# Optimization experiments

Hardware: AMD Instinct MI355X
Metric: run time of the kernel (lower is better)

## Reference

```python
import jax, jax.numpy as jnp
import numpy as np

B, T = 64, 32
F_DIM, V = 1024, 4000
H = V  # hidden_size == vocab_size in the module


def setup_inputs() -> dict:
    key = jax.random.key(0)
    ks = jax.random.split(key, 10)
    s = 1.0 / np.sqrt(H)  # torch LSTM init: U(-1/sqrt(H), 1/sqrt(H))
    u = lambda k, shp: jax.random.uniform(k, shp, jnp.float32, -s, s)
    return {
        "features": jax.random.normal(ks[0], (B, F_DIM), jnp.float32),
        "captions": jax.random.randint(ks[1], (B, T), 0, V, jnp.int32),
        "W_ih0": u(ks[2], (4 * H, F_DIM + V)),
        "W_hh0": u(ks[3], (4 * H, H)),
        "b_ih0": u(ks[4], (4 * H,)),
        "b_hh0": u(ks[5], (4 * H,)),
        "W_ih1": u(ks[6], (4 * H, H)),
        "W_hh1": u(ks[7], (4 * H, H)),
        "b_ih1": u(ks[8], (4 * H,)),
        "b_hh1": u(ks[9], (4 * H,)),
    }


def _lstm_cell(pre, h, c, W_hh, b_hh):
    # pre: precomputed input-to-hidden contribution [B, 4H]
    g = pre + h @ W_hh.T + b_hh
    i, f, gg, o = jnp.split(g, 4, axis=-1)  # torch gate order i,f,g,o
    c = jax.nn.sigmoid(f) * c + jax.nn.sigmoid(i) * jnp.tanh(gg)
    h = jax.nn.sigmoid(o) * jnp.tanh(c)
    return h, c


def reference(features, W_ih0, W_hh0, b_ih0, b_hh0, W_ih1, W_hh1, b_ih1, b_hh1, captions):
    Bb, Tt = captions.shape
    dt = features.dtype
    # Input at step t (t=1..T-1) is concat(features, onehot(captions[:, t-1])).
    # onehot @ W_v.T is a row-gather of W_v.T -> no dense onehot materialized.
    W_f = W_ih0[:, :F_DIM]            # [4H, F]
    W_v = W_ih0[:, F_DIM:]            # [4H, V]
    feat_pre = features @ W_f.T       # [B, 4H], time-invariant
    tok_pre = W_v.T[captions[:, : Tt - 1]]  # [B, T-1, 4H]
    ih0 = feat_pre[:, None, :] + tok_pre + b_ih0
    xs = jnp.swapaxes(ih0, 0, 1)      # [T-1, B, 4H]

    init = tuple(jnp.zeros((Bb, H), dt) for _ in range(4))

    def step(carry, pre0):
        h0, c0, h1, c1 = carry
        h0, c0 = _lstm_cell(pre0, h0, c0, W_hh0, b_hh0)
        pre1 = h0 @ W_ih1.T + b_ih1
        h1, c1 = _lstm_cell(pre1, h1, c1, W_hh1, b_hh1)
        return (h0, c0, h1, c1), h1

    _, ys = jax.lax.scan(step, init, xs)  # [T-1, B, H]
    # outputs[:, 0, :] stays zeros in the original (loop starts at t=1)
    outs = jnp.concatenate([jnp.zeros((Bb, 1, H), dt), jnp.swapaxes(ys, 0, 1)], axis=1)
    return outs
```

## Files before the change

kernel.cpp:

```cpp
#include <hip/hip_runtime.h>

#define DEVINL __device__ __forceinline__

typedef __attribute__((ext_vector_type(4))) float f32x4;
typedef __attribute__((ext_vector_type(8))) short s16x8;
typedef __attribute__((ext_vector_type(4))) unsigned short u16x4;
typedef __attribute__((ext_vector_type(8))) unsigned short u16x8;

static constexpr int HDIM = 4000;
static constexpr int G4   = 16000;
static constexpr int FD   = 1024;
static constexpr int LD0  = 5024;
static constexpr int TT   = 31;
static constexpr int NJ   = 64 * 31;
static constexpr int KCT  = 125;
static constexpr unsigned NBLK = 250;

DEVINL float bf2f(unsigned short u) {
  unsigned v = (unsigned)u << 16;
  return __builtin_bit_cast(float, v);
}
DEVINL unsigned short f2bf(float x) {
  unsigned u = __builtin_bit_cast(unsigned, x);
  u += 0x7fffu + ((u >> 16) & 1u);
  return (unsigned short)(u >> 16);
}
DEVINL float sigm(float x) { return 1.f / (1.f + __expf(-x)); }
DEVINL float tanh_(float x) { float e = __expf(2.f * x); return (e - 1.f) / (e + 1.f); }

#define MFMA_BF16 __builtin_amdgcn_mfma_f32_16x16x32_bf16

DEVINL s16x8 ld8p(const unsigned short* p) { return *(const s16x8*)p; }

DEVINL void mfma8r(s16x8 a0, s16x8 a1, s16x8 b0, s16x8 b1, s16x8 b2, s16x8 b3,
                   f32x4 acc[2][4]) {
  acc[0][0] = MFMA_BF16(a0, b0, acc[0][0], 0, 0, 0);
  acc[0][1] = MFMA_BF16(a0, b1, acc[0][1], 0, 0, 0);
  acc[0][2] = MFMA_BF16(a0, b2, acc[0][2], 0, 0, 0);
  acc[0][3] = MFMA_BF16(a0, b3, acc[0][3], 0, 0, 0);
  acc[1][0] = MFMA_BF16(a1, b0, acc[1][0], 0, 0, 0);
  acc[1][1] = MFMA_BF16(a1, b1, acc[1][1], 0, 0, 0);
  acc[1][2] = MFMA_BF16(a1, b2, acc[1][2], 0, 0, 0);
  acc[1][3] = MFMA_BF16(a1, b3, acc[1][3], 0, 0, 0);
}

DEVINL void gpairP(const unsigned short* __restrict__ W0,
                   const unsigned short* __restrict__ W1,
                   const unsigned short* __restrict__ hP,
                   int kc0, int kc1, int dir, int lane, int lr, int lg,
                   f32x4 acc[2][4]) {
  int n = kc1 - kc0;
  int lo = lane * 8, bo = (lg * 64 + lr) * 8;
#define KCI(s) ((size_t)(dir ? (kc1 - 1 - (s)) : (kc0 + (s))))
  s16x8 x0 = ld8p(W0 + KCI(0) * 512 + lo), x1 = ld8p(W1 + KCI(0) * 512 + lo);
  s16x8 y0 = ld8p(W0 + KCI(1) * 512 + lo), y1 = ld8p(W1 + KCI(1) * 512 + lo);
  const unsigned short* hb = hP + KCI(0) * 2048 + bo;
  s16x8 p0 = ld8p(hb), p1 = ld8p(hb + 128), p2 = ld8p(hb + 256), p3 = ld8p(hb + 384);
  int s = 0;
  for (; s + 2 <= n; s += 2) {
    hb = hP + KCI(s + 1) * 2048 + bo;
    s16x8 q0 = ld8p(hb), q1 = ld8p(hb + 128), q2 = ld8p(hb + 256), q3 = ld8p(hb + 384);
    mfma8r(x0, x1, p0, p1, p2, p3, acc);
    int s2 = (s + 2 < n) ? s + 2 : n - 1;
    x0 = ld8p(W0 + KCI(s2) * 512 + lo); x1 = ld8p(W1 + KCI(s2) * 512 + lo);
    hb = hP + KCI(s2) * 2048 + bo;
    p0 = ld8p(hb); p1 = ld8p(hb + 128); p2 = ld8p(hb + 256); p3 = ld8p(hb + 384);
    mfma8r(y0, y1, q0, q1, q2, q3, acc);
    int s3 = (s + 3 < n) ? s + 3 : n - 1;
    y0 = ld8p(W0 + KCI(s3) * 512 + lo); y1 = ld8p(W1 + KCI(s3) * 512 + lo);
  }
  if (s < n) mfma8r(x0, x1, p0, p1, p2, p3, acc);
}

DEVINL void gpair2P(const unsigned short* __restrict__ Wi0,
                    const unsigned short* __restrict__ Wi1,
                    const unsigned short* __restrict__ Wh0,
                    const unsigned short* __restrict__ Wh1,
                    const unsigned short* __restrict__ h0P,
                    const unsigned short* __restrict__ h1P,
                    int kc0, int kc1, int dir, int lane, int lr, int lg,
                    f32x4 acc[2][4]) {
  int n = kc1 - kc0;
  int lo = lane * 8, bo = (lg * 64 + lr) * 8;
  s16x8 xi0 = ld8p(Wi0 + KCI(0) * 512 + lo), xi1 = ld8p(Wi1 + KCI(0) * 512 + lo);
  s16x8 xh0 = ld8p(Wh0 + KCI(0) * 512 + lo), xh1 = ld8p(Wh1 + KCI(0) * 512 + lo);
  s16x8 yi0 = ld8p(Wi0 + KCI(1) * 512 + lo), yi1 = ld8p(Wi1 + KCI(1) * 512 + lo);
  s16x8 yh0 = ld8p(Wh0 + KCI(1) * 512 + lo), yh1 = ld8p(Wh1 + KCI(1) * 512 + lo);
  const unsigned short* hb = h0P + KCI(0) * 2048 + bo;
  s16x8 p0 = ld8p(hb), p1 = ld8p(hb + 128), p2 = ld8p(hb + 256), p3 = ld8p(hb + 384);
  int s = 0;
  for (; s + 2 <= n; s += 2) {
    hb = h1P + KCI(s) * 2048 + bo;
    s16x8 c0 = ld8p(hb), c1 = ld8p(hb + 128), c2 = ld8p(hb + 256), c3 = ld8p(hb + 384);
    mfma8r(xi0, xi1, p0, p1, p2, p3, acc);
    int s2 = (s + 2 < n) ? s + 2 : n - 1;
    xi0 = ld8p(Wi0 + KCI(s2) * 512 + lo); xi1 = ld8p(Wi1 + KCI(s2) * 512 + lo);
    hb = h0P + KCI(s + 1) * 2048 + bo;
    p0 = ld8p(hb); p1 = ld8p(hb + 128); p2 = ld8p(hb + 256); p3 = ld8p(hb + 384);
    mfma8r(xh0, xh1, c0, c1, c2, c3, acc);
    xh0 = ld8p(Wh0 + KCI(s2) * 512 + lo); xh1 = ld8p(Wh1 + KCI(s2) * 512 + lo);
    hb = h1P + KCI(s + 1) * 2048 + bo;
    c0 = ld8p(hb); c1 = ld8p(hb + 128); c2 = ld8p(hb + 256); c3 = ld8p(hb + 384);
    mfma8r(yi0, yi1, p0, p1, p2, p3, acc);
    int s3 = (s + 3 < n) ? s + 3 : n - 1;
    yi0 = ld8p(Wi0 + KCI(s3) * 512 + lo); yi1 = ld8p(Wi1 + KCI(s3) * 512 + lo);
    hb = h0P + KCI(s2) * 2048 + bo;
    p0 = ld8p(hb); p1 = ld8p(hb + 128); p2 = ld8p(hb + 256); p3 = ld8p(hb + 384);
    mfma8r(yh0, yh1, c0, c1, c2, c3, acc);
    yh0 = ld8p(Wh0 + KCI(s3) * 512 + lo); yh1 = ld8p(Wh1 + KCI(s3) * 512 + lo);
  }
  if (s < n) {
    hb = h1P + KCI(s) * 2048 + bo;
    s16x8 c0 = ld8p(hb), c1 = ld8p(hb + 128), c2 = ld8p(hb + 256), c3 = ld8p(hb + 384);
    mfma8r(xi0, xi1, p0, p1, p2, p3, acc);
    mfma8r(xh0, xh1, c0, c1, c2, c3, acc);
  }
#undef KCI
}

DEVINL void reduce_acc4(float gl[2][4][16][65], f32x4 acc[2][4],
                        int gp, int kq, int lr, int lg) {
  for (int rnd = 0; rnd < 2; ++rnd) {
    if ((kq >> 1) == rnd) {
      int slot = kq & 1;
      #pragma unroll
      for (int j = 0; j < 2; ++j) {
        int g = 2 * gp + j;
        #pragma unroll
        for (int n0 = 0; n0 < 4; ++n0)
          #pragma unroll
          for (int e = 0; e < 4; ++e) {
            float* d = &gl[slot][g][4 * lg + e][(n0 << 4) + lr];
            if (rnd == 0) *d = acc[j][n0][e];
            else          *d += acc[j][n0][e];
          }
      }
    }
    __syncthreads();
  }
}

__global__ void to_bf16_k(const float* __restrict__ s, unsigned short* __restrict__ d, long n) {
  long i = (((long)blockIdx.x * blockDim.x) + threadIdx.x) * 8;
  if (i >= n) return;
  f32x4 a = *(const f32x4*)(s + i);
  f32x4 b = *(const f32x4*)(s + i + 4);
  u16x8 o;
  o[0] = f2bf(a[0]); o[1] = f2bf(a[1]); o[2] = f2bf(a[2]); o[3] = f2bf(a[3]);
  o[4] = f2bf(b[0]); o[5] = f2bf(b[1]); o[6] = f2bf(b[2]); o[7] = f2bf(b[3]);
  *(u16x8*)(d + i) = o;
}

__global__ __launch_bounds__(256) void pack_k(const float* __restrict__ W,
                                              unsigned short* __restrict__ P) {
  int wv = (blockIdx.x << 2) + (threadIdx.x >> 6);
  int lane = threadIdx.x & 63, lr = lane & 15, lg = lane >> 4;
  int rb = wv / 500; int rem = wv - rb * 500;
  int g = rem / KCT; int kc = rem - g * KCT;
  int row = g * 4000 + rb * 16 + lr;
  int col = kc * 32 + lg * 8;
  const float* sp = W + (size_t)row * 4000 + col;
  f32x4 a = *(const f32x4*)sp;
  f32x4 b = *(const f32x4*)(sp + 4);
  u16x8 o;
  o[0] = f2bf(a[0]); o[1] = f2bf(a[1]); o[2] = f2bf(a[2]); o[3] = f2bf(a[3]);
  o[4] = f2bf(b[0]); o[5] = f2bf(b[1]); o[6] = f2bf(b[2]); o[7] = f2bf(b[3]);
  *(u16x8*)(P + ((size_t)wv * 64 + lane) * 8) = o;
}

__global__ void wf_conv_k(const float* __restrict__ s, unsigned short* __restrict__ d) {
  int idx = blockIdx.x * blockDim.x + threadIdx.x;
  int r = idx >> 7;
  int k8 = (idx & 127) << 3;
  const float* sp = s + (size_t)r * LD0 + k8;
  f32x4 a = *(const f32x4*)sp;
  f32x4 b = *(const f32x4*)(sp + 4);
  u16x8 o;
  o[0] = f2bf(a[0]); o[1] = f2bf(a[1]); o[2] = f2bf(a[2]); o[3] = f2bf(a[3]);
  o[4] = f2bf(b[0]); o[5] = f2bf(b[1]); o[6] = f2bf(b[2]); o[7] = f2bf(b[3]);
  *(u16x8*)(d + (size_t)r * FD + k8) = o;
}

DEVINL void gemm16u(const unsigned short* __restrict__ W,
                    const unsigned short* __restrict__ Hb,
                    int K, int kbeg, int kend, int lr, int lg, f32x4* acc) {
  const unsigned short* wp  = W  + (size_t)lr * K + 8 * lg + kbeg;
  const unsigned short* hp0 = Hb + (size_t)lr * K + 8 * lg + kbeg;
  const unsigned short* hp1 = hp0 + (size_t)16 * K;
  const unsigned short* hp2 = hp0 + (size_t)32 * K;
  const unsigned short* hp3 = hp0 + (size_t)48 * K;
  int nk = kend - kbeg;
  #pragma unroll 2
  for (int k = 0; k < nk; k += 32) {
    s16x8 a  = *(const s16x8*)(wp  + k);
    s16x8 b0 = *(const s16x8*)(hp0 + k);
    s16x8 b1 = *(const s16x8*)(hp1 + k);
    s16x8 b2 = *(const s16x8*)(hp2 + k);
    s16x8 b3 = *(const s16x8*)(hp3 + k);
    acc[0] = MFMA_BF16(a, b0, acc[0], 0, 0, 0);
    acc[1] = MFMA_BF16(a, b1, acc[1], 0, 0, 0);
    acc[2] = MFMA_BF16(a, b2, acc[2], 0, 0, 0);
    acc[3] = MFMA_BF16(a, b3, acc[3], 0, 0, 0);
  }
}

__global__ __launch_bounds__(512, 2) void featpre_k(
    const unsigned short* __restrict__ Wf, const unsigned short* __restrict__ Fb,
    const float* __restrict__ bih0, float* __restrict__ fp0) {
  __shared__ float gl[2][4][16][64];
  int tid = threadIdx.x, lane = tid & 63, wid = tid >> 6;
  int lr = lane & 15, lg = lane >> 4;
  int sub = wid & 3, kh = wid >> 2;
  int rowblk = blockIdx.x << 6;
  size_t row0 = (size_t)rowblk + (sub << 4);
  f32x4 acc[4] = {};
  gemm16u(Wf + row0 * FD, Fb, FD, kh ? 512 : 0, kh ? 1024 : 512, lr, lg, acc);
  #pragma unroll
  for (int n0 = 0; n0 < 4; ++n0)
    #pragma unroll
    for (int e = 0; e < 4; ++e)
      gl[kh][sub][4 * lg + e][(n0 << 4) + lr] = acc[n0][e];
  __syncthreads();
  for (int n = tid; n < 4096; n += 512) {
    int i = n & 63, b = n >> 6;
    int r = rowblk + i;
    float v = gl[0][i >> 4][i & 15][b] + gl[1][i >> 4][i & 15][b] + bih0[r];
    fp0[(size_t)b * G4 + r] = v;
  }
}

__global__ __launch_bounds__(256) void gather_k(
    const float* __restrict__ Wih0, const int* __restrict__ caps,
    const float* __restrict__ fp0, unsigned short* __restrict__ ih0T) {
  __shared__ unsigned short wv[4][4000];
  int r0 = blockIdx.x << 2;
  for (int rr = 0; rr < 4; ++rr) {
    const float* src = Wih0 + (size_t)(r0 + rr) * LD0 + FD;
    for (int c4 = threadIdx.x; c4 < 1000; c4 += 256) {
      f32x4 v = *(const f32x4*)(src + c4 * 4);
      u16x4 o;
      o[0] = f2bf(v[0]); o[1] = f2bf(v[1]); o[2] = f2bf(v[2]); o[3] = f2bf(v[3]);
      *(u16x4*)(&wv[rr][c4 * 4]) = o;
    }
  }
  __syncthreads();
  for (int j = threadIdx.x; j < NJ; j += 256) {
    int b = j / TT, t = j - b * TT;
    int tok = caps[(b << 5) + t];
    f32x4 f = *(const f32x4*)(fp0 + (size_t)b * G4 + r0);
    #pragma unroll
    for (int rr = 0; rr < 4; ++rr)
      ih0T[(size_t)(r0 + rr) * NJ + j] = f2bf(f[rr] + bf2f(wv[rr][tok]));
  }
}

__global__ __launch_bounds__(256) void tj_k(const unsigned short* __restrict__ src,
                                            unsigned short* __restrict__ dst) {
  __shared__ unsigned short tile[32][34];
  int r0 = blockIdx.x << 5;
  int j0 = blockIdx.y << 5;
  int c = threadIdx.x & 31, q = threadIdx.x >> 5;
  #pragma unroll
  for (int e = 0; e < 4; ++e) {
    int rr = q + e * 8;
    tile[rr][c] = src[(size_t)(r0 + rr) * NJ + j0 + c];
  }
  __syncthreads();
  #pragma unroll
  for (int e = 0; e < 4; ++e) {
    int jj = q + e * 8;
    dst[(size_t)(j0 + jj) * G4 + r0 + c] = tile[c][jj];
  }
}

DEVINL size_t hpk(int r, int b) {
  return ((size_t)(r >> 3) * 64 + b) * 8 + (r & 7);
}

DEVINL void gridbar3(unsigned* __restrict__ arrive, unsigned* __restrict__ go,
                     unsigned val) {
  __syncthreads();
  if (threadIdx.x == 0) {
    __builtin_amdgcn_fence(__ATOMIC_RELEASE, "agent");
    __hip_atomic_store(&arrive[blockIdx.x * 32], val, __ATOMIC_RELAXED,
                       __HIP_MEMORY_SCOPE_AGENT);
  }
  if (blockIdx.x == 0) {
    if (threadIdx.x < NBLK) {
      while (__hip_atomic_load(&arrive[threadIdx.x * 32], __ATOMIC_RELAXED,
                               __HIP_MEMORY_SCOPE_AGENT) < val) {}
    }
    __syncthreads();
    if (threadIdx.x == 0)
      __hip_atomic_store(go, val, __ATOMIC_RELAXED, __HIP_MEMORY_SCOPE_AGENT);
  } else if (threadIdx.x == 0) {
    while (__hip_atomic_load(go, __ATOMIC_RELAXED,
                             __HIP_MEMORY_SCOPE_AGENT) < val) {
      __builtin_amdgcn_s_sleep(2);
    }
  }
  if (threadIdx.x == 0)
    __builtin_amdgcn_fence(__ATOMIC_ACQUIRE, "agent");
  __syncthreads();
}

__global__ __launch_bounds__(512, 2) void lstm_persist6_k(
    const unsigned short* __restrict__ pWhh0, const unsigned short* __restrict__ pWih1,
    const unsigned short* __restrict__ pWhh1,
    unsigned short* __restrict__ h0b, unsigned short* __restrict__ h1b,
    const unsigned short* __restrict__ ih0J,
    const float* __restrict__ bhh0, const float* __restrict__ bih1,
    const float* __restrict__ bhh1, float* __restrict__ out,
    unsigned* __restrict__ bar) {
  __shared__ float gl[2][4][16][65];
  int tid = threadIdx.x, lane = tid & 63, wid = tid >> 6;
  int lr = lane & 15, lg = lane >> 4;
  int gp = wid & 1, kq = wid >> 1;
  int kc0 = (kq * KCT) >> 2, kc1 = ((kq + 1) * KCT) >> 2;
  int i = tid & 15, bb0 = tid >> 4;
  int r = (blockIdx.x << 4) + i;
  size_t wo0 = ((size_t)(blockIdx.x * 4 + 2 * gp) * KCT) * 512;
  size_t wo1 = wo0 + (size_t)KCT * 512;
  unsigned* arrive = bar;
  unsigned* go = bar + 8192;

  float c0r[2] = {0.f, 0.f}, c1r[2] = {0.f, 0.f};

  for (int p = 0; p <= TT; ++p) {
    int dir = p & 1;
    for (int half = 0; half < 2; ++half) {
      bool run_l0 = (half == dir);
      if (run_l0) {
        if (p >= TT) continue;
        const unsigned short* h0_in = h0b + (size_t)((p ^ 1) & 1) * 256000;
        unsigned short* h0_out      = h0b + (size_t)(p & 1) * 256000;
        f32x4 acc[2][4] = {};
        if (p > 0)
          gpairP(pWhh0 + wo0, pWhh0 + wo1, h0_in, kc0, kc1, dir, lane, lr, lg, acc);
        reduce_acc4(gl, acc, gp, kq, lr, lg);
        #pragma unroll
        for (int hh = 0; hh < 2; ++hh) {
          int bb = bb0 + (hh << 5);
          const unsigned short* ih = ih0J + (size_t)(bb * TT + p) * G4;
          float gi = gl[0][0][i][bb] + gl[1][0][i][bb] + bf2f(ih[r])            + bhh0[r];
          float gf = gl[0][1][i][bb] + gl[1][1][i][bb] + bf2f(ih[HDIM + r])     + bhh0[HDIM + r];
          float gg = gl[0][2][i][bb] + gl[1][2][i][bb] + bf2f(ih[2 * HDIM + r]) + bhh0[2 * HDIM + r];
          float go_ = gl[0][3][i][bb] + gl[1][3][i][bb] + bf2f(ih[3 * HDIM + r]) + bhh0[3 * HDIM + r];
          c0r[hh] = sigm(gf) * c0r[hh] + sigm(gi) * tanh_(gg);
          float hn = sigm(go_) * tanh_(c0r[hh]);
          h0_out[hpk(r, bb)] = f2bf(hn);
        }
        __syncthreads();
      } else {
        if (p < 1) continue;
        int t = p - 1;
        const unsigned short* h0_t  = h0b + (size_t)(t & 1) * 256000;
        const unsigned short* h1_in = h1b + (size_t)((t ^ 1) & 1) * 256000;
        unsigned short* h1_out      = h1b + (size_t)(t & 1) * 256000;
        f32x4 acc[2][4] = {};
        if (t > 0)
          gpair2P(pWih1 + wo0, pWih1 + wo1, pWhh1 + wo0, pWhh1 + wo1,
                  h0_t, h1_in, kc0, kc1, dir, lane, lr, lg, acc);
        else
          gpairP(pWih1 + wo0, pWih1 + wo1, h0_t, kc0, kc1, dir, lane, lr, lg, acc);
        reduce_acc4(gl, acc, gp, kq, lr, lg);
        #pragma unroll
        for (int hh = 0; hh < 2; ++hh) {
          int bb = bb0 + (hh << 5);
          float gi = gl[0][0][i][bb] + gl[1][0][i][bb] + bih1[r]            + bhh1[r];
          float gf = gl[0][1][i][bb] + gl[1][1][i][bb] + bih1[HDIM + r]     + bhh1[HDIM + r];
          float gg = gl[0][2][i][bb] + gl[1][2][i][bb] + bih1[2 * HDIM + r] + bhh1[2 * HDIM + r];
          float go_ = gl[0][3][i][bb] + gl[1][3][i][bb] + bih1[3 * HDIM + r] + bhh1[3 * HDIM + r];
          c1r[hh] = sigm(gf) * c1r[hh] + sigm(gi) * tanh_(gg);
          float hn = sigm(go_) * tanh_(c1r[hh]);
          h1_out[hpk(r, bb)] = f2bf(hn);
          out[(size_t)bb * (32 * HDIM) + (size_t)(t + 1) * HDIM + r] = hn;
        }
        __syncthreads();
      }
    }
    if (p < TT) gridbar3(arrive, go, (unsigned)(p + 1));
  }
}

__global__ void sentinel_k(float* o) { o[0] = -123456.f; }

extern "C" void kernel_launch(void* const* d_in, const int* in_sizes, int n_in,
                              void* d_out, int out_size, void* d_ws, size_t ws_size,
                              hipStream_t stream) {
  (void)in_sizes; (void)n_in;
  const float* features = (const float*)d_in[0];
  const int*   captions = (const int*)d_in[1];
  const float* W_ih0    = (const float*)d_in[2];
  const float* W_hh0    = (const float*)d_in[3];
  const float* b_ih0    = (const float*)d_in[4];
  const float* b_hh0    = (const float*)d_in[5];
  const float* W_ih1    = (const float*)d_in[6];
  const float* W_hh1    = (const float*)d_in[7];
  const float* b_ih1    = (const float*)d_in[8];
  const float* b_hh1    = (const float*)d_in[9];
  float* out = (float*)d_out;

  char* w = (char*)d_ws;
  unsigned short* h0b   = (unsigned short*)(w);
  unsigned short* h1b   = (unsigned short*)(w + 1024000);
  unsigned short* pWhh0 = (unsigned short*)(w + 4096000);
  unsigned short* pWih1 = (unsigned short*)(w + 132096000);
  unsigned short* pWhh1 = (unsigned short*)(w + 260096000);
  unsigned short* bWf   = (unsigned short*)(w + 388096000);
  unsigned short* ih0T  = (unsigned short*)(w + 420864000);
  float*          fp0   = (float*)(w + 484352000);
  unsigned short* bFeat = (unsigned short*)(w + 488448000);
  unsigned short* ih0J  = (unsigned short*)(w + 488579328);
  unsigned*       bar   = (unsigned*)(w + 552067328);
  const size_t NEED = 552104192;
  if (ws_size < NEED) { sentinel_k<<<1, 1, 0, stream>>>(out); return; }

  hipMemsetAsync(d_out, 0, (size_t)out_size * 4, stream);
  hipMemsetAsync(w + 552067328, 0, 36864, stream);

  pack_k<<<31250, 256, 0, stream>>>(W_hh0, pWhh0);
  pack_k<<<31250, 256, 0, stream>>>(W_ih1, pWih1);
  pack_k<<<31250, 256, 0, stream>>>(W_hh1, pWhh1);
  to_bf16_k<<<32,    256, 0, stream>>>(features, bFeat, 65536L);
  wf_conv_k<<<8000,  256, 0, stream>>>(W_ih0, bWf);
  featpre_k<<<250,   512, 0, stream>>>(bWf, bFeat, b_ih0, fp0);
  gather_k<<<4000,   256, 0, stream>>>(W_ih0, captions, fp0, ih0T);
  tj_k<<<dim3(500, 62), 256, 0, stream>>>(ih0T, ih0J);

  lstm_persist6_k<<<NBLK, 512, 0, stream>>>(pWhh0, pWih1, pWhh1, h0b, h1b,
                                            ih0J, b_hh0, b_ih1, b_hh1, out, bar);
}
```

Measured before the change: 2.970 ms.

## Replace persistent grid-barrier LSTM kernel with per-step launches running both layers concurrently

```diff
diff --git a/kernel.cpp b/kernel.cpp
--- a/kernel.cpp
+++ b/kernel.cpp
@@ -14,7 +14,6 @@
 static constexpr int TT   = 31;
 static constexpr int NJ   = 64 * 31;
 static constexpr int KCT  = 125;
-static constexpr unsigned NBLK = 250;
 
 DEVINL float bf2f(unsigned short u) {
   unsigned v = (unsigned)u << 16;
@@ -277,109 +276,76 @@
   return ((size_t)(r >> 3) * 64 + b) * 8 + (r & 7);
 }
 
-DEVINL void gridbar3(unsigned* __restrict__ arrive, unsigned* __restrict__ go,
-                     unsigned val) {
-  __syncthreads();
-  if (threadIdx.x == 0) {
-    __builtin_amdgcn_fence(__ATOMIC_RELEASE, "agent");
-    __hip_atomic_store(&arrive[blockIdx.x * 32], val, __ATOMIC_RELAXED,
-                       __HIP_MEMORY_SCOPE_AGENT);
-  }
-  if (blockIdx.x == 0) {
-    if (threadIdx.x < NBLK) {
-      while (__hip_atomic_load(&arrive[threadIdx.x * 32], __ATOMIC_RELAXED,
-                               __HIP_MEMORY_SCOPE_AGENT) < val) {}
-    }
-    __syncthreads();
-    if (threadIdx.x == 0)
-      __hip_atomic_store(go, val, __ATOMIC_RELAXED, __HIP_MEMORY_SCOPE_AGENT);
-  } else if (threadIdx.x == 0) {
-    while (__hip_atomic_load(go, __ATOMIC_RELAXED,
-                             __HIP_MEMORY_SCOPE_AGENT) < val) {
-      __builtin_amdgcn_s_sleep(2);
-    }
-  }
-  if (threadIdx.x == 0)
-    __builtin_amdgcn_fence(__ATOMIC_ACQUIRE, "agent");
-  __syncthreads();
-}
-
-__global__ __launch_bounds__(512, 2) void lstm_persist6_k(
+__global__ __launch_bounds__(512, 2) void step_lr_k(
     const unsigned short* __restrict__ pWhh0, const unsigned short* __restrict__ pWih1,
     const unsigned short* __restrict__ pWhh1,
     unsigned short* __restrict__ h0b, unsigned short* __restrict__ h1b,
+    float* __restrict__ c0, float* __restrict__ c1,
     const unsigned short* __restrict__ ih0J,
     const float* __restrict__ bhh0, const float* __restrict__ bih1,
-    const float* __restrict__ bhh1, float* __restrict__ out,
-    unsigned* __restrict__ bar) {
+    const float* __restrict__ bhh1, float* __restrict__ out, int p) {
   __shared__ float gl[2][4][16][65];
+  bool is_l1 = blockIdx.x >= 250;
+  int rb = is_l1 ? (int)blockIdx.x - 250 : (int)blockIdx.x;
   int tid = threadIdx.x, lane = tid & 63, wid = tid >> 6;
   int lr = lane & 15, lg = lane >> 4;
   int gp = wid & 1, kq = wid >> 1;
   int kc0 = (kq * KCT) >> 2, kc1 = ((kq + 1) * KCT) >> 2;
+  int dir = p & 1;
   int i = tid & 15, bb0 = tid >> 4;
-  int r = (blockIdx.x << 4) + i;
-  size_t wo0 = ((size_t)(blockIdx.x * 4 + 2 * gp) * KCT) * 512;
+  int r = (rb << 4) + i;
+  size_t wo0 = ((size_t)(rb * 4 + 2 * gp) * KCT) * 512;
   size_t wo1 = wo0 + (size_t)KCT * 512;
-  unsigned* arrive = bar;
-  unsigned* go = bar + 8192;
-
-  float c0r[2] = {0.f, 0.f}, c1r[2] = {0.f, 0.f};
-
-  for (int p = 0; p <= TT; ++p) {
-    int dir = p & 1;
-    for (int half = 0; half < 2; ++half) {
-      bool run_l0 = (half == dir);
-      if (run_l0) {
-        if (p >= TT) continue;
-        const unsigned short* h0_in = h0b + (size_t)((p ^ 1) & 1) * 256000;
-        unsigned short* h0_out      = h0b + (size_t)(p & 1) * 256000;
-        f32x4 acc[2][4] = {};
-        if (p > 0)
-          gpairP(pWhh0 + wo0, pWhh0 + wo1, h0_in, kc0, kc1, dir, lane, lr, lg, acc);
-        reduce_acc4(gl, acc, gp, kq, lr, lg);
-        #pragma unroll
-        for (int hh = 0; hh < 2; ++hh) {
-          int bb = bb0 + (hh << 5);
-          const unsigned short* ih = ih0J + (size_t)(bb * TT + p) * G4;
-          float gi = gl[0][0][i][bb] + gl[1][0][i][bb] + bf2f(ih[r])            + bhh0[r];
-          float gf = gl[0][1][i][bb] + gl[1][1][i][bb] + bf2f(ih[HDIM + r])     + bhh0[HDIM + r];
-          float gg = gl[0][2][i][bb] + gl[1][2][i][bb] + bf2f(ih[2 * HDIM + r]) + bhh0[2 * HDIM + r];
-          float go_ = gl[0][3][i][bb] + gl[1][3][i][bb] + bf2f(ih[3 * HDIM + r]) + bhh0[3 * HDIM + r];
-          c0r[hh] = sigm(gf) * c0r[hh] + sigm(gi) * tanh_(gg);
-          float hn = sigm(go_) * tanh_(c0r[hh]);
-          h0_out[hpk(r, bb)] = f2bf(hn);
-        }
-        __syncthreads();
-      } else {
-        if (p < 1) continue;
-        int t = p - 1;
-        const unsigned short* h0_t  = h0b + (size_t)(t & 1) * 256000;
-        const unsigned short* h1_in = h1b + (size_t)((t ^ 1) & 1) * 256000;
-        unsigned short* h1_out      = h1b + (size_t)(t & 1) * 256000;
-        f32x4 acc[2][4] = {};
-        if (t > 0)
-          gpair2P(pWih1 + wo0, pWih1 + wo1, pWhh1 + wo0, pWhh1 + wo1,
-                  h0_t, h1_in, kc0, kc1, dir, lane, lr, lg, acc);
-        else
-          gpairP(pWih1 + wo0, pWih1 + wo1, h0_t, kc0, kc1, dir, lane, lr, lg, acc);
-        reduce_acc4(gl, acc, gp, kq, lr, lg);
-        #pragma unroll
-        for (int hh = 0; hh < 2; ++hh) {
-          int bb = bb0 + (hh << 5);
-          float gi = gl[0][0][i][bb] + gl[1][0][i][bb] + bih1[r]            + bhh1[r];
-          float gf = gl[0][1][i][bb] + gl[1][1][i][bb] + bih1[HDIM + r]     + bhh1[HDIM + r];
-          float gg = gl[0][2][i][bb] + gl[1][2][i][bb] + bih1[2 * HDIM + r] + bhh1[2 * HDIM + r];
-          float go_ = gl[0][3][i][bb] + gl[1][3][i][bb] + bih1[3 * HDIM + r] + bhh1[3 * HDIM + r];
-          c1r[hh] = sigm(gf) * c1r[hh] + sigm(gi) * tanh_(gg);
-          float hn = sigm(go_) * tanh_(c1r[hh]);
-          h1_out[hpk(r, bb)] = f2bf(hn);
-          out[(size_t)bb * (32 * HDIM) + (size_t)(t + 1) * HDIM + r] = hn;
-        }
-        __syncthreads();
-      }
+
+  if (!is_l1) {
+    if (p >= TT) return;
+    const unsigned short* h0_in = h0b + (size_t)((p ^ 1) & 1) * 256000;
+    unsigned short* h0_out      = h0b + (size_t)(p & 1) * 256000;
+    f32x4 acc[2][4] = {};
+    if (p > 0)
+      gpairP(pWhh0 + wo0, pWhh0 + wo1, h0_in, kc0, kc1, dir, lane, lr, lg, acc);
+    reduce_acc4(gl, acc, gp, kq, lr, lg);
+    #pragma unroll
+    for (int hh = 0; hh < 2; ++hh) {
+      int bb = bb0 + (hh << 5);
+      size_t ci = (size_t)bb * HDIM + r;
+      const unsigned short* ih = ih0J + (size_t)(bb * TT + p) * G4;
+      float gi = gl[0][0][i][bb] + gl[1][0][i][bb] + bf2f(ih[r])            + bhh0[r];
+      float gf = gl[0][1][i][bb] + gl[1][1][i][bb] + bf2f(ih[HDIM + r])     + bhh0[HDIM + r];
+      float gg = gl[0][2][i][bb] + gl[1][2][i][bb] + bf2f(ih[2 * HDIM + r]) + bhh0[2 * HDIM + r];
+      float go_ = gl[0][3][i][bb] + gl[1][3][i][bb] + bf2f(ih[3 * HDIM + r]) + bhh0[3 * HDIM + r];
+      float cn = sigm(gf) * c0[ci] + sigm(gi) * tanh_(gg);
+      float hn = sigm(go_) * tanh_(cn);
+      c0[ci] = cn;
+      h0_out[hpk(r, bb)] = f2bf(hn);
     }
-    if (p < TT) gridbar3(arrive, go, (unsigned)(p + 1));
+  } else {
+    int t = p - 1;
+    if (t < 0) return;
+    const unsigned short* h0_t  = h0b + (size_t)(t & 1) * 256000;
+    const unsigned short* h1_in = h1b + (size_t)((t ^ 1) & 1) * 256000;
+    unsigned short* h1_out      = h1b + (size_t)(t & 1) * 256000;
+    f32x4 acc[2][4] = {};
+    if (t > 0)
+      gpair2P(pWih1 + wo0, pWih1 + wo1, pWhh1 + wo0, pWhh1 + wo1,
+              h0_t, h1_in, kc0, kc1, dir, lane, lr, lg, acc);
+    else
+      gpairP(pWih1 + wo0, pWih1 + wo1, h0_t, kc0, kc1, dir, lane, lr, lg, acc);
+    reduce_acc4(gl, acc, gp, kq, lr, lg);
+    #pragma unroll
+    for (int hh = 0; hh < 2; ++hh) {
+      int bb = bb0 + (hh << 5);
+      size_t ci = (size_t)bb * HDIM + r;
+      float gi = gl[0][0][i][bb] + gl[1][0][i][bb] + bih1[r]            + bhh1[r];
+      float gf = gl[0][1][i][bb] + gl[1][1][i][bb] + bih1[HDIM + r]     + bhh1[HDIM + r];
+      float gg = gl[0][2][i][bb] + gl[1][2][i][bb] + bih1[2 * HDIM + r] + bhh1[2 * HDIM + r];
+      float go_ = gl[0][3][i][bb] + gl[1][3][i][bb] + bih1[3 * HDIM + r] + bhh1[3 * HDIM + r];
+      float cn = sigm(gf) * c1[ci] + sigm(gi) * tanh_(gg);
+      float hn = sigm(go_) * tanh_(cn);
+      c1[ci] = cn;
+      h1_out[hpk(r, bb)] = f2bf(hn);
+      out[(size_t)bb * (32 * HDIM) + (size_t)(t + 1) * HDIM + r] = hn;
+    }
   }
 }
 
@@ -404,6 +370,8 @@
   char* w = (char*)d_ws;
   unsigned short* h0b   = (unsigned short*)(w);
   unsigned short* h1b   = (unsigned short*)(w + 1024000);
+  float*          c0    = (float*)(w + 2048000);
+  float*          c1    = (float*)(w + 3072000);
   unsigned short* pWhh0 = (unsigned short*)(w + 4096000);
   unsigned short* pWih1 = (unsigned short*)(w + 132096000);
   unsigned short* pWhh1 = (unsigned short*)(w + 260096000);
@@ -412,12 +380,11 @@
   float*          fp0   = (float*)(w + 484352000);
   unsigned short* bFeat = (unsigned short*)(w + 488448000);
   unsigned short* ih0J  = (unsigned short*)(w + 488579328);
-  unsigned*       bar   = (unsigned*)(w + 552067328);
-  const size_t NEED = 552104192;
+  const size_t NEED = 552067328;
   if (ws_size < NEED) { sentinel_k<<<1, 1, 0, stream>>>(out); return; }
 
   hipMemsetAsync(d_out, 0, (size_t)out_size * 4, stream);
-  hipMemsetAsync(w + 552067328, 0, 36864, stream);
+  hipMemsetAsync(w, 0, 4096000, stream);
 
   pack_k<<<31250, 256, 0, stream>>>(W_hh0, pWhh0);
   pack_k<<<31250, 256, 0, stream>>>(W_ih1, pWih1);
@@ -428,6 +395,8 @@
   gather_k<<<4000,   256, 0, stream>>>(W_ih0, captions, fp0, ih0T);
   tj_k<<<dim3(500, 62), 256, 0, stream>>>(ih0T, ih0J);
 
-  lstm_persist6_k<<<NBLK, 512, 0, stream>>>(pWhh0, pWih1, pWhh1, h0b, h1b,
-                                            ih0J, b_hh0, b_ih1, b_hh1, out, bar);
-}
+  for (int p = 0; p <= TT; ++p) {
+    step_lr_k<<<500, 512, 0, stream>>>(pWhh0, pWih1, pWhh1, h0b, h1b, c0, c1,
+                                       ih0J, b_hh0, b_ih1, b_hh1, out, p);
+  }
+}
```

Result: faster. 2.876 ms (-3.2%).
